# Performance work log

Hardware: AMD Instinct MI355X
Metric: run time of the kernel (lower is better)

Reference implementation:

```python
import jax, jax.numpy as jnp
import numpy as np

B, T, A = 64, 100, 8732          # batch, padded GT boxes per image, SSD300 anchors
NUM_CLASSES = 21                 # VOC
THR = 0.5                        # overlap_threshold
VAR0, VAR1 = 0.1, 0.2            # loc_variance


def setup_inputs() -> dict:
    key = jax.random.key(0)
    k1, k2, k3, k4, k5 = jax.random.split(key, 5)
    # GT boxes: valid point-coord boxes in [0,1] with positive area, plus float label col
    xy1 = jax.random.uniform(k1, (B, T, 2)) * 0.7
    wh = jax.random.uniform(k2, (B, T, 2)) * 0.28 + 0.02
    labels = jax.random.randint(k3, (B, T), 0, NUM_CLASSES - 1).astype(jnp.float32)
    targets = jnp.concatenate([xy1, xy1 + wh, labels[..., None]], axis=-1)  # [B,T,5]
    # anchors in center coords (cx, cy, w, h), positive w/h
    cxy = jax.random.uniform(k4, (A, 2))
    awh = jax.random.uniform(k5, (A, 2)) * 0.48 + 0.02
    anchors = jnp.concatenate([cxy, awh], axis=-1)  # [A,4]
    return {"targets": targets, "anchors": anchors}


def _iou(boxes, anchors_pt):
    # boxes [T,4] point coords, anchors_pt [A,4] point coords -> [T,A]
    tl = jnp.maximum(boxes[:, None, :2], anchors_pt[None, :, :2])
    br = jnp.minimum(boxes[:, None, 2:], anchors_pt[None, :, 2:])
    inter = jnp.prod(jnp.clip(br - tl, 0.0), axis=-1)
    area_b = jnp.prod(boxes[:, 2:] - boxes[:, :2], axis=-1)
    area_a = jnp.prod(anchors_pt[:, 2:] - anchors_pt[:, :2], axis=-1)
    return inter / (area_b[:, None] + area_a[None, :] - inter)


def reference(targets, anchors):
    # centerCoordsToPointCoords(anchors)
    anchors_pt = jnp.concatenate(
        [anchors[:, :2] - anchors[:, 2:] * 0.5, anchors[:, :2] + anchors[:, 2:] * 0.5],
        axis=-1,
    )

    def match(tgt):  # tgt: [T,5]
        boxes = tgt[:, :4]
        labels = tgt[:, 4]
        iou = _iou(boxes, anchors_pt)                    # [T,A]
        anchor_index = jnp.argmax(iou, axis=1)           # best anchor per GT [T]
        gt_overlap = jnp.max(iou, axis=0)                # best GT overlap per anchor [A]
        gt_index = jnp.argmax(iou, axis=0)               # best GT per anchor [A]
        # index_fill_: guarantee each GT's best anchor counts as matched
        gt_overlap = gt_overlap.at[anchor_index].set(1.0)
        gt_index = gt_index.at[anchor_index].set(jnp.arange(boxes.shape[0]))
        matched = boxes[gt_index]                        # [A,4] point coords
        # pointCoordsToCenterCoords + encodeCenterCoords
        cxy = (matched[:, :2] + matched[:, 2:]) * 0.5
        wh = matched[:, 2:] - matched[:, :2]
        loc = jnp.concatenate(
            [(cxy - anchors[:, :2]) / (VAR0 * anchors[:, 2:]),
             jnp.log(wh / anchors[:, 2:]) / VAR1],
            axis=-1,
        )                                                # [A,4]
        conf = (labels[gt_index] + 1.0).astype(jnp.int32)
        conf = jnp.where(gt_overlap < THR, 0, conf)      # background below threshold
        return loc, conf

    return jax.vmap(match)(targets)  # loc_t [B,A,4], conf_t [B,A]
```

## Files before the change

kernel.cpp:

```cpp
#include <hip/hip_runtime.h>

#define BB 64
#define TT 100
#define AA 8732
#define CHUNK 512
#define NCHUNK ((AA + CHUNK - 1) / CHUNK)

typedef unsigned long long u64;
typedef unsigned int u32;
typedef unsigned short u16;

__constant__ int c_tbl[5] = {0, 28, 52, 76, 100};

__device__ __forceinline__ float fdiv_faithful(float i, float u) {
    float r = __builtin_amdgcn_rcpf(u);
    r = __builtin_fmaf(__builtin_fmaf(-u, r, 1.0f), r, r);
    float q = __fmul_rn(i, r);
    float rem = __builtin_fmaf(-u, q, i);
    return __builtin_fmaf(rem, r, q);
}

__device__ __forceinline__ float iou_f(float bx1, float by1, float bx2, float by2, float areab,
                                       float ax1, float ay1, float ax2, float ay2, float areaa) {
    float dx = fmaxf(__fsub_rn(fminf(bx2, ax2), fmaxf(bx1, ax1)), 0.0f);
    float dy = fmaxf(__fsub_rn(fminf(by2, ay2), fmaxf(by1, ay1)), 0.0f);
    float inter = __fmul_rn(dx, dy);
    float uni = __fsub_rn(__fadd_rn(areab, areaa), inter);
    return fdiv_faithful(inter, uni);
}

__device__ __forceinline__ void wave_max63_x4(float& x0, float& x1, float& x2, float& x3) {
    asm volatile(
        "s_nop 1\n\t"
        "v_max_f32 %0, %0, %0 row_shr:1\n\t"
        "v_max_f32 %1, %1, %1 row_shr:1\n\t"
        "v_max_f32 %2, %2, %2 row_shr:1\n\t"
        "v_max_f32 %3, %3, %3 row_shr:1\n\t"
        "v_max_f32 %0, %0, %0 row_shr:2\n\t"
        "v_max_f32 %1, %1, %1 row_shr:2\n\t"
        "v_max_f32 %2, %2, %2 row_shr:2\n\t"
        "v_max_f32 %3, %3, %3 row_shr:2\n\t"
        "v_max_f32 %0, %0, %0 row_shr:4\n\t"
        "v_max_f32 %1, %1, %1 row_shr:4\n\t"
        "v_max_f32 %2, %2, %2 row_shr:4\n\t"
        "v_max_f32 %3, %3, %3 row_shr:4\n\t"
        "v_max_f32 %0, %0, %0 row_shr:8\n\t"
        "v_max_f32 %1, %1, %1 row_shr:8\n\t"
        "v_max_f32 %2, %2, %2 row_shr:8\n\t"
        "v_max_f32 %3, %3, %3 row_shr:8\n\t"
        "v_max_f32 %0, %0, %0 row_bcast:15\n\t"
        "v_max_f32 %1, %1, %1 row_bcast:15\n\t"
        "v_max_f32 %2, %2, %2 row_bcast:15\n\t"
        "v_max_f32 %3, %3, %3 row_bcast:15\n\t"
        "v_max_f32 %0, %0, %0 row_bcast:31\n\t"
        "v_max_f32 %1, %1, %1 row_bcast:31\n\t"
        "v_max_f32 %2, %2, %2 row_bcast:31\n\t"
        "v_max_f32 %3, %3, %3 row_bcast:31\n\t"
        "s_nop 0"
        : "+v"(x0), "+v"(x1), "+v"(x2), "+v"(x3));
}

__global__ __launch_bounds__(256) void k_init(u64* __restrict__ keys) {
    int i = blockIdx.x * 256 + threadIdx.x;
    if (i < BB * TT) keys[i] = 0ULL;
}

__global__ __launch_bounds__(512) void k_phaseA(const float* __restrict__ targets,
                                                const float* __restrict__ anchors,
                                                u64* __restrict__ keys,
                                                u64* __restrict__ pa2) {
    const int b = blockIdx.y;
    const int z = blockIdx.z;
    const int tid = threadIdx.x;
    const int half = tid >> 8;
    const int u = tid & 255;
    const int a0 = blockIdx.x * CHUNK + u * 2;
    const bool valid = a0 < AA;
    const int lane = tid & 63, wv = tid >> 6;

    __shared__ float4 sh_box[TT];
    __shared__ __align__(16) float sh_area[TT];
    __shared__ u64 sh_red[4][TT];
    __shared__ u64 sh_pa[CHUNK];

    if (tid < TT) {
        const float* tg = targets + ((size_t)b * TT + tid) * 5;
        float x1 = tg[0], y1 = tg[1], x2 = tg[2], y2 = tg[3];
        sh_box[tid] = make_float4(x1, y1, x2, y2);
        sh_area[tid] = __fmul_rn(__fsub_rn(x2, x1), __fsub_rn(y2, y1));
    }
    __syncthreads();

    float ax10 = 0.f, ay10 = 0.f, ax20 = 0.f, ay20 = 0.f, aa0 = 1.f;
    float ax11 = 0.f, ay11 = 0.f, ax21 = 0.f, ay21 = 0.f, aa1 = 1.f;
    if (valid) {
        const float4* anc = (const float4*)(anchors + (size_t)a0 * 4);
        float4 c0 = anc[0], c1 = anc[1];
        float hx0 = __fmul_rn(c0.z, 0.5f), hy0 = __fmul_rn(c0.w, 0.5f);
        ax10 = __fsub_rn(c0.x, hx0); ay10 = __fsub_rn(c0.y, hy0);
        ax20 = __fadd_rn(c0.x, hx0); ay20 = __fadd_rn(c0.y, hy0);
        aa0 = __fmul_rn(__fsub_rn(ax20, ax10), __fsub_rn(ay20, ay10));
        float hx1 = __fmul_rn(c1.z, 0.5f), hy1 = __fmul_rn(c1.w, 0.5f);
        ax11 = __fsub_rn(c1.x, hx1); ay11 = __fsub_rn(c1.y, hy1);
        ax21 = __fadd_rn(c1.x, hx1); ay21 = __fadd_rn(c1.y, hy1);
        aa1 = __fmul_rn(__fsub_rn(ax21, ax11), __fsub_rn(ay21, ay11));
    }

    float best0 = -1.f, best1 = -1.f;
    int gi0 = 0, gi1 = 0;
    const u32 wave_base = (u32)blockIdx.x * CHUNK + (u32)(wv & 3) * 128u;

    const int tbeg = c_tbl[z * 2 + half];
    const int tend = c_tbl[z * 2 + half + 1];
    for (int t = tbeg; t < tend; t += 4) {
        float4 B0 = sh_box[t + 0], B1 = sh_box[t + 1];
        float4 B2 = sh_box[t + 2], B3 = sh_box[t + 3];
        const float4 arv = *(const float4*)&sh_area[t];
        float ar0 = arv.x, ar1 = arv.y, ar2 = arv.z, ar3 = arv.w;

        float v00 = iou_f(B0.x, B0.y, B0.z, B0.w, ar0, ax10, ay10, ax20, ay20, aa0);
        float v01 = iou_f(B0.x, B0.y, B0.z, B0.w, ar0, ax11, ay11, ax21, ay21, aa1);
        float v10 = iou_f(B1.x, B1.y, B1.z, B1.w, ar1, ax10, ay10, ax20, ay20, aa0);
        float v11 = iou_f(B1.x, B1.y, B1.z, B1.w, ar1, ax11, ay11, ax21, ay21, aa1);
        float v20 = iou_f(B2.x, B2.y, B2.z, B2.w, ar2, ax10, ay10, ax20, ay20, aa0);
        float v21 = iou_f(B2.x, B2.y, B2.z, B2.w, ar2, ax11, ay11, ax21, ay21, aa1);
        float v30 = iou_f(B3.x, B3.y, B3.z, B3.w, ar3, ax10, ay10, ax20, ay20, aa0);
        float v31 = iou_f(B3.x, B3.y, B3.z, B3.w, ar3, ax11, ay11, ax21, ay21, aa1);

        if (v00 > best0) { best0 = v00; gi0 = t; }
        if (v10 > best0) { best0 = v10; gi0 = t + 1; }
        if (v20 > best0) { best0 = v20; gi0 = t + 2; }
        if (v30 > best0) { best0 = v30; gi0 = t + 3; }
        if (v01 > best1) { best1 = v01; gi1 = t; }
        if (v11 > best1) { best1 = v11; gi1 = t + 1; }
        if (v21 > best1) { best1 = v21; gi1 = t + 2; }
        if (v31 > best1) { best1 = v31; gi1 = t + 3; }

        float vm0 = fmaxf(v00, v01), vm1 = fmaxf(v10, v11);
        float vm2 = fmaxf(v20, v21), vm3 = fmaxf(v30, v31);
        float w0 = vm0, w1 = vm1, w2 = vm2, w3 = vm3;
        wave_max63_x4(w0, w1, w2, w3);
        u32 wm0 = (u32)__builtin_amdgcn_readlane(__float_as_int(w0), 63);
        u32 wm1 = (u32)__builtin_amdgcn_readlane(__float_as_int(w1), 63);
        u32 wm2 = (u32)__builtin_amdgcn_readlane(__float_as_int(w2), 63);
        u32 wm3 = (u32)__builtin_amdgcn_readlane(__float_as_int(w3), 63);
        u64 me0 = __ballot(vm0 == __uint_as_float(wm0));
        u64 mp0 = __ballot(v01 > v00);
        u64 me1 = __ballot(vm1 == __uint_as_float(wm1));
        u64 mp1 = __ballot(v11 > v10);
        u64 me2 = __ballot(vm2 == __uint_as_float(wm2));
        u64 mp2 = __ballot(v21 > v20);
        u64 me3 = __ballot(vm3 == __uint_as_float(wm3));
        u64 mp3 = __ballot(v31 > v30);
        u32 wl0 = (u32)(__ffsll((long long)me0) - 1);
        u32 wl1 = (u32)(__ffsll((long long)me1) - 1);
        u32 wl2 = (u32)(__ffsll((long long)me2) - 1);
        u32 wl3 = (u32)(__ffsll((long long)me3) - 1);
        u32 g0 = wave_base + wl0 * 2u + (u32)((mp0 >> wl0) & 1ULL);
        u32 g1 = wave_base + wl1 * 2u + (u32)((mp1 >> wl1) & 1ULL);
        u32 g2 = wave_base + wl2 * 2u + (u32)((mp2 >> wl2) & 1ULL);
        u32 g3 = wave_base + wl3 * 2u + (u32)((mp3 >> wl3) & 1ULL);
        if (lane == 0) {
            u64* r = &sh_red[wv & 3][t];
            r[0] = (((u64)wm0) << 32) | (u32)~g0;
            r[1] = (((u64)wm1) << 32) | (u32)~g1;
            r[2] = (((u64)wm2) << 32) | (u32)~g2;
            r[3] = (((u64)wm3) << 32) | (u32)~g3;
        }
    }
    __syncthreads();

    if (tid >= c_tbl[z * 2] && tid < c_tbl[z * 2 + 2]) {
        u64 m0 = sh_red[0][tid], m1 = sh_red[1][tid];
        u64 m2 = sh_red[2][tid], m3 = sh_red[3][tid];
        u64 m = m0 > m1 ? m0 : m1;
        if (m2 > m) m = m2;
        if (m3 > m) m = m3;
        atomicMax(&keys[b * TT + tid], m);
    }

    if (half == 0) {
        sh_pa[u * 2 + 0] = (((u64)__float_as_uint(best0)) << 32) | (u32)(~(u32)gi0);
        sh_pa[u * 2 + 1] = (((u64)__float_as_uint(best1)) << 32) | (u32)(~(u32)gi1);
    }
    __syncthreads();
    if (half == 1 && valid) {
        u64 k0 = (((u64)__float_as_uint(best0)) << 32) | (u32)(~(u32)gi0);
        u64 k1 = (((u64)__float_as_uint(best1)) << 32) | (u32)(~(u32)gi1);
        u64 m0 = sh_pa[u * 2 + 0]; if (k0 > m0) m0 = k0;
        u64 m1 = sh_pa[u * 2 + 1]; if (k1 > m1) m1 = k1;
        pa2[((size_t)b * AA + a0) * 2 + z] = m0;
        pa2[((size_t)b * AA + a0 + 1) * 2 + z] = m1;
    }
}

__global__ __launch_bounds__(256) void k_encode(const float* __restrict__ targets,
                                                const float* __restrict__ anchors,
                                                const u64* __restrict__ keys,
                                                const u64* pa2,
                                                float* out) {
    const int b = blockIdx.y;
    const int a = blockIdx.x * 256 + threadIdx.x;

    __shared__ float sh_t[TT][6];
    __shared__ u32 sh_ov[256];

    sh_ov[threadIdx.x] = 0;
    __syncthreads();
    for (int t = threadIdx.x; t < TT; t += 256) {
        const float* tg = targets + ((size_t)b * TT + t) * 5;
        sh_t[t][0] = tg[0]; sh_t[t][1] = tg[1];
        sh_t[t][2] = tg[2]; sh_t[t][3] = tg[3];
        sh_t[t][4] = tg[4];
        u32 at = ~(u32)(keys[b * TT + t] & 0xFFFFFFFFu);
        if ((at >> 8) == (u32)blockIdx.x)
            atomicMax(&sh_ov[at & 255], 0x100u | (u32)t);
    }
    __syncthreads();
    if (a >= AA) return;

    const u64* pc = pa2 + ((size_t)b * AA + a) * 2;
    u64 kz0 = pc[0], kz1 = pc[1];
    u64 m = kz0 > kz1 ? kz0 : kz1;

    u32 ov = sh_ov[threadIdx.x];
    int gi; bool pos;
    if (ov) { gi = (int)(ov & 0x7F); pos = true; }
    else {
        gi = (int)((~(u32)m) & 0x7F);
        pos = __uint_as_float((u32)(m >> 32)) >= 0.5f;
    }

    const float4 anc = *(const float4*)(anchors + (size_t)a * 4);
    const float mx1 = sh_t[gi][0], my1 = sh_t[gi][1], mx2 = sh_t[gi][2], my2 = sh_t[gi][3];
    const float cx = (mx1 + mx2) * 0.5f, cy = (my1 + my2) * 0.5f;
    const float w = mx2 - mx1, h = my2 - my1;
    const float l0 = (cx - anc.x) / (0.1f * anc.z);
    const float l1 = (cy - anc.y) / (0.1f * anc.w);
    const float l2 = logf(w / anc.z) / 0.2f;
    const float l3 = logf(h / anc.w) / 0.2f;

    const size_t base = ((size_t)b * AA + a) * 4;
    *(float4*)(out + base) = make_float4(l0, l1, l2, l3);
    float conf = pos ? (float)(int)(sh_t[gi][4] + 1.0f) : 0.0f;
    out[(size_t)BB * AA * 4 + (size_t)b * AA + a] = conf;
}

extern "C" void kernel_launch(void* const* d_in, const int* in_sizes, int n_in,
                              void* d_out, int out_size, void* d_ws, size_t ws_size,
                              hipStream_t stream) {
    const float* targets = (const float*)d_in[0];
    const float* anchors = (const float*)d_in[1];
    float* out = (float*)d_out;
    u64* keys = (u64*)d_ws;
    u64* pa2 = (u64*)d_out;

    k_init<<<(BB * TT + 255) / 256, 256, 0, stream>>>(keys);
    dim3 gA(NCHUNK, BB, 2);
    k_phaseA<<<gA, 512, 0, stream>>>(targets, anchors, keys, pa2);
    dim3 gE((AA + 255) / 256, BB);
    k_encode<<<gE, 256, 0, stream>>>(targets, anchors, keys, pa2, out);
}
```

Before: 109.7 us.

## Split GT range into five z-slices with atomicMax merge of per-anchor best

Replaces the 512-thread blocks (two halves over two GT sub-ranges each, merged in shared memory) with 256-thread blocks over five 20-GT slices. Per-anchor best IoU keys are merged across slices with global 64-bit atomicMax into a single slot, so the init kernel must now zero that slot for every anchor. The encoder reads one key instead of two. This aims for more blocks and shorter per-block loops, at the cost of extra atomics, a larger init kernel and redundant anchor loads. It also adds a clamp to 1 on the overlap width and height, which does not change results for boxes inside [0,1].

Result: slower. 129.0 us (+17.5%).

```diff
diff --git a/kernel.cpp b/kernel.cpp
--- a/kernel.cpp
+++ b/kernel.cpp
@@ -5,12 +5,13 @@
 #define AA 8732
 #define CHUNK 512
 #define NCHUNK ((AA + CHUNK - 1) / CHUNK)
+#define NZ 5
 
 typedef unsigned long long u64;
 typedef unsigned int u32;
 typedef unsigned short u16;
 
-__constant__ int c_tbl[5] = {0, 28, 52, 76, 100};
+__constant__ int c_tbl[NZ + 1] = {0, 20, 40, 60, 80, 100};
 
 __device__ __forceinline__ float fdiv_faithful(float i, float u) {
     float r = __builtin_amdgcn_rcpf(u);
@@ -22,8 +23,8 @@
 
 __device__ __forceinline__ float iou_f(float bx1, float by1, float bx2, float by2, float areab,
                                        float ax1, float ay1, float ax2, float ay2, float areaa) {
-    float dx = fmaxf(__fsub_rn(fminf(bx2, ax2), fmaxf(bx1, ax1)), 0.0f);
-    float dy = fmaxf(__fsub_rn(fminf(by2, ay2), fmaxf(by1, ay1)), 0.0f);
+    float dx = fminf(fmaxf(__fsub_rn(fminf(bx2, ax2), fmaxf(bx1, ax1)), 0.0f), 1.0f);
+    float dy = fminf(fmaxf(__fsub_rn(fminf(by2, ay2), fmaxf(by1, ay1)), 0.0f), 1.0f);
     float inter = __fmul_rn(dx, dy);
     float uni = __fsub_rn(__fadd_rn(areab, areaa), inter);
     return fdiv_faithful(inter, uni);
@@ -60,28 +61,26 @@
         : "+v"(x0), "+v"(x1), "+v"(x2), "+v"(x3));
 }
 
-__global__ __launch_bounds__(256) void k_init(u64* __restrict__ keys) {
+__global__ __launch_bounds__(256) void k_init(u64* __restrict__ keys, u64* __restrict__ pa2) {
     int i = blockIdx.x * 256 + threadIdx.x;
     if (i < BB * TT) keys[i] = 0ULL;
-}
-
-__global__ __launch_bounds__(512) void k_phaseA(const float* __restrict__ targets,
+    if (i < BB * AA) pa2[(size_t)i * 2] = 0ULL;
+}
+
+__global__ __launch_bounds__(256) void k_phaseA(const float* __restrict__ targets,
                                                 const float* __restrict__ anchors,
                                                 u64* __restrict__ keys,
                                                 u64* __restrict__ pa2) {
     const int b = blockIdx.y;
     const int z = blockIdx.z;
     const int tid = threadIdx.x;
-    const int half = tid >> 8;
-    const int u = tid & 255;
-    const int a0 = blockIdx.x * CHUNK + u * 2;
+    const int a0 = blockIdx.x * CHUNK + tid * 2;
     const bool valid = a0 < AA;
     const int lane = tid & 63, wv = tid >> 6;
 
     __shared__ float4 sh_box[TT];
     __shared__ __align__(16) float sh_area[TT];
     __shared__ u64 sh_red[4][TT];
-    __shared__ u64 sh_pa[CHUNK];
 
     if (tid < TT) {
         const float* tg = targets + ((size_t)b * TT + tid) * 5;
@@ -108,10 +107,10 @@
 
     float best0 = -1.f, best1 = -1.f;
     int gi0 = 0, gi1 = 0;
-    const u32 wave_base = (u32)blockIdx.x * CHUNK + (u32)(wv & 3) * 128u;
-
-    const int tbeg = c_tbl[z * 2 + half];
-    const int tend = c_tbl[z * 2 + half + 1];
+    const u32 wave_base = (u32)blockIdx.x * CHUNK + (u32)wv * 128u;
+
+    const int tbeg = c_tbl[z];
+    const int tend = c_tbl[z + 1];
     for (int t = tbeg; t < tend; t += 4) {
         float4 B0 = sh_box[t + 0], B1 = sh_box[t + 1];
         float4 B2 = sh_box[t + 2], B3 = sh_box[t + 3];
@@ -161,7 +160,7 @@
         u32 g2 = wave_base + wl2 * 2u + (u32)((mp2 >> wl2) & 1ULL);
         u32 g3 = wave_base + wl3 * 2u + (u32)((mp3 >> wl3) & 1ULL);
         if (lane == 0) {
-            u64* r = &sh_red[wv & 3][t];
+            u64* r = &sh_red[wv][t];
             r[0] = (((u64)wm0) << 32) | (u32)~g0;
             r[1] = (((u64)wm1) << 32) | (u32)~g1;
             r[2] = (((u64)wm2) << 32) | (u32)~g2;
@@ -170,7 +169,7 @@
     }
     __syncthreads();
 
-    if (tid >= c_tbl[z * 2] && tid < c_tbl[z * 2 + 2]) {
+    if (tid >= tbeg && tid < tend) {
         u64 m0 = sh_red[0][tid], m1 = sh_red[1][tid];
         u64 m2 = sh_red[2][tid], m3 = sh_red[3][tid];
         u64 m = m0 > m1 ? m0 : m1;
@@ -179,18 +178,11 @@
         atomicMax(&keys[b * TT + tid], m);
     }
 
-    if (half == 0) {
-        sh_pa[u * 2 + 0] = (((u64)__float_as_uint(best0)) << 32) | (u32)(~(u32)gi0);
-        sh_pa[u * 2 + 1] = (((u64)__float_as_uint(best1)) << 32) | (u32)(~(u32)gi1);
-    }
-    __syncthreads();
-    if (half == 1 && valid) {
+    if (valid) {
         u64 k0 = (((u64)__float_as_uint(best0)) << 32) | (u32)(~(u32)gi0);
         u64 k1 = (((u64)__float_as_uint(best1)) << 32) | (u32)(~(u32)gi1);
-        u64 m0 = sh_pa[u * 2 + 0]; if (k0 > m0) m0 = k0;
-        u64 m1 = sh_pa[u * 2 + 1]; if (k1 > m1) m1 = k1;
-        pa2[((size_t)b * AA + a0) * 2 + z] = m0;
-        pa2[((size_t)b * AA + a0 + 1) * 2 + z] = m1;
+        atomicMax(&pa2[((size_t)b * AA + a0) * 2], k0);
+        atomicMax(&pa2[((size_t)b * AA + a0 + 1) * 2], k1);
     }
 }
 
@@ -219,9 +211,7 @@
     __syncthreads();
     if (a >= AA) return;
 
-    const u64* pc = pa2 + ((size_t)b * AA + a) * 2;
-    u64 kz0 = pc[0], kz1 = pc[1];
-    u64 m = kz0 > kz1 ? kz0 : kz1;
+    const u64 m = pa2[((size_t)b * AA + a) * 2];
 
     u32 ov = sh_ov[threadIdx.x];
     int gi; bool pos;
@@ -255,9 +245,9 @@
     u64* keys = (u64*)d_ws;
     u64* pa2 = (u64*)d_out;
 
-    k_init<<<(BB * TT + 255) / 256, 256, 0, stream>>>(keys);
-    dim3 gA(NCHUNK, BB, 2);
-    k_phaseA<<<gA, 512, 0, stream>>>(targets, anchors, keys, pa2);
+    k_init<<<(BB * AA + 255) / 256, 256, 0, stream>>>(keys, pa2);
+    dim3 gA(NCHUNK, BB, NZ);
+    k_phaseA<<<gA, 256, 0, stream>>>(targets, anchors, keys, pa2);
     dim3 gE((AA + 255) / 256, BB);
     k_encode<<<gE, 256, 0, stream>>>(targets, anchors, keys, pa2, out);
 }
```
